# Kernel tuning notes

Hardware: AMD Instinct MI355X
Metric: run time of the kernel (lower is better)

Reference implementation:

```python
import jax, jax.numpy as jnp
import numpy as np

L, B, S, D, H, F, V = 6, 4, 512, 768, 12, 3072, 30522
DH = D // H
EPS = 1e-12
SCALE = 1.0 / float(np.sqrt(DH))


def _ln(x, g, b):
    m = jnp.mean(x, axis=-1, keepdims=True)
    v = jnp.mean(jnp.square(x - m), axis=-1, keepdims=True)
    return (x - m) * jax.lax.rsqrt(v + EPS) * g + b


def _mha(xq, xkv, Wq, bq, Wk, bk, Wv, bv, causal):
    Bc, Sq, _ = xq.shape
    Sk = xkv.shape[1]
    q = (xq @ Wq + bq).reshape(Bc, Sq, H, DH).transpose(0, 2, 1, 3)
    k = (xkv @ Wk + bk).reshape(Bc, Sk, H, DH).transpose(0, 2, 1, 3)
    v = (xkv @ Wv + bv).reshape(Bc, Sk, H, DH).transpose(0, 2, 1, 3)
    s = jnp.einsum('bhqd,bhkd->bhqk', q, k) * SCALE
    if causal is not None:
        s = jnp.where(causal[None, None], s, -jnp.inf)
    p = jax.nn.softmax(s, axis=-1)
    ctx = jnp.einsum('bhqk,bhkd->bhqd', p, v)
    return ctx.transpose(0, 2, 1, 3).reshape(Bc, Sq, H * DH)


def _fwd(input_ids, encoder_hidden, word_emb, pos_emb, tok_emb, emb_g, emb_b,
         Wq, bq, Wk, bk, Wv, bv, Wo, bo, ln1_g, ln1_b,
         cWq, cbq, cWk, cbk, cWv, cbv, cWo, cbo, ln2_g, ln2_b,
         Wi, bi, Wf, bf, ln3_g, ln3_b,
         Wt, bt, lnh_g, lnh_b, Wdec, bdec):
    Bc, Sc = input_ids.shape
    # BertEmbeddings: word + position + token_type(all zeros) -> LayerNorm
    h = word_emb[input_ids] + pos_emb[:Sc][None] + tok_emb[0][None, None]
    h = _ln(h, emb_g, emb_b)
    causal = jnp.tril(jnp.ones((Sc, Sc), dtype=bool))
    for l in range(L):
        # causal self-attention + residual LayerNorm
        ctx = _mha(h, h, Wq[l], bq[l], Wk[l], bk[l], Wv[l], bv[l], causal)
        h = _ln(h + ctx @ Wo[l] + bo[l], ln1_g[l], ln1_b[l])
        # cross-attention over encoder_hidden (no mask) + residual LayerNorm
        ctx = _mha(h, encoder_hidden, cWq[l], cbq[l], cWk[l], cbk[l], cWv[l], cbv[l], None)
        h = _ln(h + ctx @ cWo[l] + cbo[l], ln2_g[l], ln2_b[l])
        # FFN (erf-gelu) + residual LayerNorm
        ff = jax.nn.gelu(h @ Wi[l] + bi[l], approximate=False) @ Wf[l] + bf[l]
        h = _ln(h + ff, ln3_g[l], ln3_b[l])
    # BertOnlyMLMHead: transform (dense+gelu+LN) then vocab projection
    t = _ln(jax.nn.gelu(h @ Wt + bt, approximate=False), lnh_g, lnh_b)
    return t @ Wdec + bdec


def setup_inputs() -> dict:
    keys = iter(jax.random.split(jax.random.key(0), 64))
    def rn(shape, s=0.02):
        return jax.random.normal(next(keys), shape, jnp.float32) * s
    inp = {
        'input_ids': jax.random.randint(next(keys), (B, S), 0, V),
        'encoder_hidden': jax.random.normal(next(keys), (B, S, D), jnp.float32),
        'word_emb': rn((V, D)), 'pos_emb': rn((S, D)), 'tok_emb': rn((2, D)),
        'emb_g': jnp.ones((D,), jnp.float32), 'emb_b': jnp.zeros((D,), jnp.float32),
        'Wq': rn((L, D, D)), 'bq': jnp.zeros((L, D), jnp.float32),
        'Wk': rn((L, D, D)), 'bk': jnp.zeros((L, D), jnp.float32),
        'Wv': rn((L, D, D)), 'bv': jnp.zeros((L, D), jnp.float32),
        'Wo': rn((L, D, D)), 'bo': jnp.zeros((L, D), jnp.float32),
        'ln1_g': jnp.ones((L, D), jnp.float32), 'ln1_b': jnp.zeros((L, D), jnp.float32),
        'cWq': rn((L, D, D)), 'cbq': jnp.zeros((L, D), jnp.float32),
        'cWk': rn((L, D, D)), 'cbk': jnp.zeros((L, D), jnp.float32),
        'cWv': rn((L, D, D)), 'cbv': jnp.zeros((L, D), jnp.float32),
        'cWo': rn((L, D, D)), 'cbo': jnp.zeros((L, D), jnp.float32),
        'ln2_g': jnp.ones((L, D), jnp.float32), 'ln2_b': jnp.zeros((L, D), jnp.float32),
        'Wi': rn((L, D, F)), 'bi': jnp.zeros((L, F), jnp.float32),
        'Wf': rn((L, F, D)), 'bf': jnp.zeros((L, D), jnp.float32),
        'ln3_g': jnp.ones((L, D), jnp.float32), 'ln3_b': jnp.zeros((L, D), jnp.float32),
        'Wt': rn((D, D)), 'bt': jnp.zeros((D,), jnp.float32),
        'lnh_g': jnp.ones((D,), jnp.float32), 'lnh_b': jnp.zeros((D,), jnp.float32),
        'Wdec': rn((D, V)), 'bdec': jnp.zeros((V,), jnp.float32),
    }
    return inp


def reference(input_ids, encoder_hidden, word_emb, pos_emb, tok_emb, emb_g, emb_b,
              Wq, bq, Wk, bk, Wv, bv, Wo, bo, ln1_g, ln1_b,
              cWq, cbq, cWk, cbk, cWv, cbv, cWo, cbo, ln2_g, ln2_b,
              Wi, bi, Wf, bf, ln3_g, ln3_b,
              Wt, bt, lnh_g, lnh_b, Wdec, bdec):
    return _fwd(input_ids, encoder_hidden, word_emb, pos_emb, tok_emb, emb_g, emb_b,
                Wq, bq, Wk, bk, Wv, bv, Wo, bo, ln1_g, ln1_b,
                cWq, cbq, cWk, cbk, cWv, cbv, cWo, cbo, ln2_g, ln2_b,
                Wi, bi, Wf, bf, ln3_g, ln3_b,
                Wt, bt, lnh_g, lnh_b, Wdec, bdec)
```

## Files before the change

### kernel.cpp

```cpp
#include <hip/hip_runtime.h>
#include <math.h>

typedef unsigned short u16;
typedef unsigned int   u32;
typedef long long      i64;
typedef __attribute__((ext_vector_type(8))) __bf16 bf16x8;
typedef __attribute__((ext_vector_type(4))) float  f32x4;
typedef __attribute__((ext_vector_type(8))) u16    u16x8;
typedef __attribute__((ext_vector_type(4))) u16    u16x4;

#define LN_EPS 1e-12f

__device__ __forceinline__ float b2f(u16 u){ union {u32 i; float f;} v; v.i = ((u32)u)<<16; return v.f; }
__device__ __forceinline__ u16 f2b(float f){ union {float f; u32 i;} v; v.f = f; u32 r = v.i + 0x7FFFu + ((v.i>>16)&1u); return (u16)(r>>16); }

__device__ __forceinline__ void gl2lds16(const u16* g, u16* l) {
  __builtin_amdgcn_global_load_lds((const __attribute__((address_space(1))) void*)g,
                                   (__attribute__((address_space(3))) void*)l, 16, 0, 0);
}

struct GemmArgs {
  const u16* A; const u16* Bt; void* C;
  const float* bias0; const float* bias1; const float* bias2;
  int lda, ldb, ldc, M, N, K, bias_seg, act, cf32;
};

template<int BM, int BN, int WM, int WN>
__global__ __launch_bounds__(WM*WN*64)
void gemm_bt2(GemmArgs g) {
  constexpr int NTHR = WM*WN*64;
  constexpr int MI = BM/(WM*16);
  constexpr int NJ = BN/(WN*16);
  constexpr int RA = (BM*4)/NTHR;
  constexpr int RB = (BN*4)/NTHR;
  __shared__ u16 As[2][BM*32];
  __shared__ u16 Bs[2][BN*32];
  const int tid  = threadIdx.x;
  const int wave = tid >> 6, lane = tid & 63;
  const int wm = wave / WN, wn = wave % WN;
  const int lrow = lane & 15, quad = lane >> 4;

  int bx, by;
  {
    const int gx = gridDim.x;
    const int nwg = gx * gridDim.y;
    const int wg = blockIdx.y * gx + blockIdx.x;
    if (nwg >= 512) {
      const int q = nwg >> 3, r = nwg & 7;
      const int xcd = wg & 7, loc = wg >> 3;
      const int nid = (xcd < r ? xcd * (q + 1) : r * (q + 1) + (xcd - r) * q) + loc;
      bx = nid % gx; by = nid / gx;
    } else { bx = blockIdx.x; by = blockIdx.y; }
  }

  const u16* Ab = g.A + (i64)bx*BM*g.lda;
  const u16* Bt = g.Bt;
  const int n0 = by * BN;

  const int srow = tid >> 2;
  const int sps  = tid & 3;

  f32x4 acc[MI][NJ];
  #pragma unroll
  for (int i=0;i<MI;i++)
    #pragma unroll
    for (int j=0;j<NJ;j++) acc[i][j] = (f32x4){0.f,0.f,0.f,0.f};

  auto stage = [&](int buf, int k0) {
    #pragma unroll
    for (int la=0; la<RA; ++la) {
      int row = la*(NTHR>>2) + srow;
      int ls = sps ^ ((row>>1)&3);
      const u16* src = Ab + (i64)row*g.lda + k0 + (ls<<3);
      gl2lds16(src, &As[buf][(la*NTHR + (wave<<6))<<3]);
    }
    #pragma unroll
    for (int la=0; la<RB; ++la) {
      int row = la*(NTHR>>2) + srow;
      int nrow = n0 + row; if (nrow >= g.N) nrow = g.N-1;
      int ls = sps ^ ((row>>1)&3);
      const u16* src = Bt + (i64)nrow*g.ldb + k0 + (ls<<3);
      gl2lds16(src, &Bs[buf][(la*NTHR + (wave<<6))<<3]);
    }
  };

  const int NT = g.K >> 5;
  stage(0, 0);
  __syncthreads();
  for (int t = 0; t < NT; ++t) {
    const int cur = t & 1;
    if (t+1 < NT) stage(cur^1, (t+1)<<5);
    const int xr = (lrow>>1)&3;
    bf16x8 a[MI], b[NJ];
    #pragma unroll
    for (int i=0;i<MI;i++) {
      int r = wm*(MI*16) + i*16 + lrow;
      a[i] = *(const bf16x8*)&As[cur][r*32 + ((quad^xr)<<3)];
    }
    #pragma unroll
    for (int j=0;j<NJ;j++) {
      int r = wn*(NJ*16) + j*16 + lrow;
      b[j] = *(const bf16x8*)&Bs[cur][r*32 + ((quad^xr)<<3)];
    }
    #pragma unroll
    for (int i=0;i<MI;i++)
      #pragma unroll
      for (int j=0;j<NJ;j++)
        acc[i][j] = __builtin_amdgcn_mfma_f32_16x16x32_bf16(a[i], b[j], acc[i][j], 0,0,0);
    __syncthreads();
  }

  const i64 rowbase = (i64)bx*BM + wm*(MI*16);
  u16*   Cb = (u16*)g.C;
  float* Cf = (float*)g.C;
  #pragma unroll
  for (int i=0;i<MI;i++) {
    #pragma unroll
    for (int j=0;j<NJ;j++) {
      int col = n0 + wn*(NJ*16) + (j<<4) + lrow;
      if (col < g.N) {
        float bias = 0.f;
        if (g.bias0) {
          int seg = col / g.bias_seg;
          const float* bp = (seg==0) ? g.bias0 : ((seg==1) ? g.bias1 : g.bias2);
          bias = bp[col - seg*g.bias_seg];
        }
        #pragma unroll
        for (int r=0;r<4;r++) {
          i64 row = rowbase + (i<<4) + (quad<<2) + r;
          float v = acc[i][j][r] + bias;
          if (g.act == 1) v = 0.5f*v*(1.0f + erff(v*0.70710678118654752f));
          if (g.cf32) Cf[row*(i64)g.ldc + col] = v;
          else        Cb[row*(i64)g.ldc + col] = f2b(v);
        }
      }
    }
  }
}

__global__ __launch_bounds__(64) void flash_attn(const u16* __restrict__ qkv,
                                                 const u16* __restrict__ VT,
                                                 u16* __restrict__ ctx, int causal) {
  const int lane = threadIdx.x & 63;
  const int qi = lane & 15, g = lane >> 4;
  const int q0 = blockIdx.x << 4;
  const int bh = blockIdx.y;
  const int b = bh / 12, h = bh % 12;
  const int q = q0 + qi;

  const u16* Qp = qkv + (i64)(b*512 + q)*2304 + h*64 + (g<<3);
  bf16x8 qf0 = *(const bf16x8*)Qp;
  bf16x8 qf1 = *(const bf16x8*)(Qp + 32);

  const u16* Kp = qkv + ((i64)(b*512 + qi))*2304 + 768 + h*64 + (g<<3);
  const u16* Vp = VT + (i64)bh*32768 + (i64)qi*512 + (g<<3);

  f32x4 o[4];
  #pragma unroll
  for (int s=0;s<4;s++) o[s] = (f32x4){0.f,0.f,0.f,0.f};
  float m = -1e30f, lsum = 0.f;

  const int sA = qi + ((g & 1) << 5);
  const int sB = sA + 16;
  const int tsel = g >> 1;

  const int nt = causal ? (q0 >> 6) + 1 : 8;
  for (int kt = 0; kt < nt; ++kt) {
    const int kv0 = kt << 6;

    bf16x8 kf[4][2];
    #pragma unroll
    for (int t=0;t<4;t++)
      #pragma unroll
      for (int w=0;w<2;w++)
        kf[t][w] = *(const bf16x8*)(Kp + (i64)(kv0 + (t<<4))*2304 + (w<<5));
    bf16x8 vf[4][2];
    #pragma unroll
    for (int s=0;s<4;s++)
      #pragma unroll
      for (int w=0;w<2;w++)
        vf[s][w] = *(const bf16x8*)(Vp + (s<<13) + kv0 + (w<<5));

    f32x4 sc[4];
    #pragma unroll
    for (int t=0;t<4;t++) {
      sc[t] = (f32x4){0.f,0.f,0.f,0.f};
      sc[t] = __builtin_amdgcn_mfma_f32_16x16x32_bf16(kf[t][0], qf0, sc[t], 0,0,0);
      sc[t] = __builtin_amdgcn_mfma_f32_16x16x32_bf16(kf[t][1], qf1, sc[t], 0,0,0);
    }

    float x[4][4];
    #pragma unroll
    for (int t=0;t<4;t++)
      #pragma unroll
      for (int r=0;r<4;r++) {
        float v = sc[t][r] * 0.125f;
        int key = kv0 + (t<<4) + (g<<2) + r;
        if (causal && key > q) v = -1e30f;
        x[t][r] = v;
      }

    float mt = x[0][0];
    #pragma unroll
    for (int t=0;t<4;t++)
      #pragma unroll
      for (int r=0;r<4;r++) mt = fmaxf(mt, x[t][r]);
    mt = fmaxf(mt, __shfl_xor(mt, 16));
    mt = fmaxf(mt, __shfl_xor(mt, 32));
    float mn = fmaxf(m, mt);
    float c = __expf(m - mn);
    m = mn;

    float p[4][4];
    float ps = 0.f;
    #pragma unroll
    for (int t=0;t<4;t++)
      #pragma unroll
      for (int r=0;r<4;r++) { float e = __expf(x[t][r] - mn); p[t][r] = e; ps += e; }
    ps += __shfl_xor(ps, 16);
    ps += __shfl_xor(ps, 32);
    lsum = lsum * c + ps;
    #pragma unroll
    for (int s=0;s<4;s++) o[s] *= c;

    u32 pkLo[4], pkHi[4];
    #pragma unroll
    for (int t=0;t<4;t++) {
      pkLo[t] = (u32)f2b(p[t][0]) | ((u32)f2b(p[t][1]) << 16);
      pkHi[t] = (u32)f2b(p[t][2]) | ((u32)f2b(p[t][3]) << 16);
    }

    #pragma unroll
    for (int w=0;w<2;w++) {
      u32 w0=0, w1=0, w2=0, w3=0;
      #pragma unroll
      for (int tl=0; tl<2; ++tl) {
        const int t = 2*w + tl;
        u32 aLo = (u32)__shfl((int)pkLo[t], sA);
        u32 aHi = (u32)__shfl((int)pkHi[t], sA);
        u32 bLo = (u32)__shfl((int)pkLo[t], sB);
        u32 bHi = (u32)__shfl((int)pkHi[t], sB);
        if (tsel == tl) { w0=aLo; w1=aHi; w2=bLo; w3=bHi; }
      }
      union { bf16x8 v; u32 u[4]; } pf;
      pf.u[0]=w0; pf.u[1]=w1; pf.u[2]=w2; pf.u[3]=w3;
      #pragma unroll
      for (int s=0;s<4;s++)
        o[s] = __builtin_amdgcn_mfma_f32_16x16x32_bf16(vf[s][w], pf.v, o[s], 0,0,0);
    }
  }

  float inv = 1.0f / lsum;
  u16* orow = ctx + (i64)(b*512 + q)*768 + h*64 + (g<<2);
  #pragma unroll
  for (int s=0;s<4;s++) {
    u16x4 ov;
    #pragma unroll
    for (int r=0;r<4;r++) ov[r] = f2b(o[s][r] * inv);
    *(u16x4*)(orow + (s<<4)) = ov;
  }
}

__device__ __forceinline__ float block_reduce_sum_256(float v, float* red) {
  #pragma unroll
  for (int off=32; off; off>>=1) v += __shfl_xor(v, off);
  int wave = threadIdx.x >> 6;
  __syncthreads();
  if ((threadIdx.x & 63) == 0) red[wave] = v;
  __syncthreads();
  return red[0]+red[1]+red[2]+red[3];
}

__global__ __launch_bounds__(256) void resln_kernel(const float* base, const float* delta,
                                                    const float* gam, const float* bet,
                                                    float* out_f, u16* out_b) {
  __shared__ float red[4];
  i64 off = (i64)blockIdx.x * 768;
  int tid = threadIdx.x;
  float x[3];
  #pragma unroll
  for (int j=0;j<3;j++) {
    int i = tid + j*256;
    float v = delta[off+i];
    if (base) v += base[off+i];
    x[j] = v;
  }
  float s = block_reduce_sum_256(x[0]+x[1]+x[2], red);
  float mean = s * (1.0f/768.0f);
  float q = 0.f;
  #pragma unroll
  for (int j=0;j<3;j++) { float d = x[j]-mean; q += d*d; }
  q = block_reduce_sum_256(q, red);
  float r = rsqrtf(q*(1.0f/768.0f) + LN_EPS);
  #pragma unroll
  for (int j=0;j<3;j++) {
    int i = tid + j*256;
    float y = (x[j]-mean)*r*gam[i] + bet[i];
    out_f[off+i] = y;
    out_b[off+i] = f2b(y);
  }
}

__global__ __launch_bounds__(256) void embed_kernel(const int* ids, const float* wemb,
    const float* pemb, const float* temb, const float* gam, const float* bet,
    float* out_f, u16* out_b) {
  __shared__ float red[4];
  int row = blockIdx.x;
  int s = row & 511;
  i64 wrow = (i64)ids[row] * 768;
  i64 off = (i64)row * 768;
  int tid = threadIdx.x;
  float x[3];
  #pragma unroll
  for (int j=0;j<3;j++) {
    int i = tid + j*256;
    x[j] = wemb[wrow+i] + pemb[(i64)s*768+i] + temb[i];
  }
  float sm = block_reduce_sum_256(x[0]+x[1]+x[2], red);
  float mean = sm * (1.0f/768.0f);
  float q = 0.f;
  #pragma unroll
  for (int j=0;j<3;j++) { float d = x[j]-mean; q += d*d; }
  q = block_reduce_sum_256(q, red);
  float r = rsqrtf(q*(1.0f/768.0f) + LN_EPS);
  #pragma unroll
  for (int j=0;j<3;j++) {
    int i = tid + j*256;
    float y = (x[j]-mean)*r*gam[i] + bet[i];
    out_f[off+i] = y;
    out_b[off+i] = f2b(y);
  }
}

__global__ __launch_bounds__(256) void cvt_kernel(const float* src, u16* dst, int n) {
  int i = (blockIdx.x*256 + threadIdx.x) * 4;
  if (i + 3 < n) {
    float4 v = *(const float4*)&src[i];
    dst[i+0]=f2b(v.x); dst[i+1]=f2b(v.y); dst[i+2]=f2b(v.z); dst[i+3]=f2b(v.w);
  }
}

struct TransEntry { const float* src; u16* dst; int K, N, tile0; };
struct TransArgs  { TransEntry e[12]; int n; };

__global__ __launch_bounds__(256) void transpose_multi(TransArgs ta) {
  __shared__ u16 tile[64][72];
  int t = blockIdx.x;
  int ei = 0;
  for (int i=1;i<ta.n;i++) if (t >= ta.e[i].tile0) ei = i;
  TransEntry E = ta.e[ei];
  int lt = t - E.tile0;
  int ntn = (E.N + 63) >> 6;
  int tk = lt / ntn, tn = lt - tk*ntn;
  int tid = threadIdx.x;
  int kk = tid >> 2, c = (tid & 3) << 4;
  i64 gk = (i64)(tk*64 + kk);
  int gn0 = tn*64 + c;
  const float* srow = E.src + gk * E.N;
  if (gn0 + 16 <= E.N) {
    #pragma unroll
    for (int j=0;j<16;j++) tile[kk][c+j] = f2b(srow[gn0+j]);
  } else {
    for (int j=0;j<16;j++) tile[kk][c+j] = (gn0+j < E.N) ? f2b(srow[gn0+j]) : (u16)0;
  }
  __syncthreads();
  int nn = tid >> 2, kc = (tid & 3) << 4;
  int gn = tn*64 + nn;
  if (gn < E.N) {
    u16x8 v0, v1;
    #pragma unroll
    for (int j=0;j<8;j++) { v0[j] = tile[kc+j][nn]; v1[j] = tile[kc+8+j][nn]; }
    u16* drow = E.dst + (i64)gn*E.K + tk*64 + kc;
    *(u16x8*)&drow[0] = v0;
    *(u16x8*)&drow[8] = v1;
  }
}

__global__ __launch_bounds__(256) void vtrans_kernel(const u16* qkv, u16* VT) {
  __shared__ u16 tile[64][72];
  int bh = blockIdx.z; int b = bh / 12, hh = bh % 12;
  const u16* src = qkv + (i64)b*512*2304 + 1536 + hh*64;
  u16* dst = VT + (i64)bh*64*512;
  int kt = blockIdx.x;
  int tid = threadIdx.x;
  int kk = tid >> 2, c = (tid & 3) << 4;
  const u32* p = (const u32*)&src[(i64)(kt*64+kk)*2304 + c];
  #pragma unroll
  for (int j=0;j<8;j++) *(u32*)&tile[kk][c + 2*j] = p[j];
  __syncthreads();
  int dd = tid >> 2, kc = (tid & 3) << 4;
  u16x8 v0, v1;
  #pragma unroll
  for (int j=0;j<8;j++) { v0[j] = tile[kc+j][dd]; v1[j] = tile[kc+8+j][dd]; }
  u16* drow = dst + (i64)dd*512 + kt*64 + kc;
  *(u16x8*)&drow[0] = v0;
  *(u16x8*)&drow[8] = v1;
}

static void gemm_args(GemmArgs& g, const u16* A, int lda, const u16* Bt, int ldb,
                      void* C, int ldc, int M, int N, int K, const float* b0,
                      const float* b1, const float* b2, int bias_seg, int act, int cf32) {
  g.A=A; g.Bt=Bt; g.C=C; g.bias0=b0; g.bias1=b1; g.bias2=b2;
  g.lda=lda; g.ldb=ldb; g.ldc=ldc; g.M=M; g.N=N; g.K=K;
  g.bias_seg=bias_seg; g.act=act; g.cf32=cf32;
}

static void g2_128(const u16* A, int lda, const u16* Bt, int ldb, void* C, int ldc,
                   int M, int N, int K, const float* b0, const float* b1, const float* b2,
                   int bias_seg, int act, int cf32, hipStream_t st) {
  GemmArgs g; gemm_args(g, A, lda, Bt, ldb, C, ldc, M, N, K, b0, b1, b2, bias_seg, act, cf32);
  gemm_bt2<128,128,2,2><<<dim3(M/128, (N+127)/128), 256, 0, st>>>(g);
}

static void g2_64(const u16* A, int lda, const u16* Bt, int ldb, void* C, int ldc,
                  int M, int N, int K, const float* b0, const float* b1, const float* b2,
                  int bias_seg, int act, int cf32, hipStream_t st) {
  GemmArgs g; gemm_args(g, A, lda, Bt, ldb, C, ldc, M, N, K, b0, b1, b2, bias_seg, act, cf32);
  gemm_bt2<64,128,1,2><<<dim3(M/64, (N+127)/128), 128, 0, st>>>(g);
}

static void g2_256(const u16* A, int lda, const u16* Bt, int ldb, void* C, int ldc,
                   int M, int N, int K, const float* b0, const float* b1, const float* b2,
                   int bias_seg, int act, int cf32, hipStream_t st) {
  GemmArgs g; gemm_args(g, A, lda, Bt, ldb, C, ldc, M, N, K, b0, b1, b2, bias_seg, act, cf32);
  gemm_bt2<256,256,2,4><<<dim3(M/256, (N+255)/256), 512, 0, st>>>(g);
}

extern "C" void kernel_launch(void* const* d_in, const int* in_sizes, int n_in,
                              void* d_out, int out_size, void* d_ws, size_t ws_size,
                              hipStream_t stream) {
  (void)in_sizes; (void)n_in; (void)out_size;
  const int*   ids  = (const int*)d_in[0];
  const float* enc  = (const float*)d_in[1];
  const float* wemb = (const float*)d_in[2];
  const float* pemb = (const float*)d_in[3];
  const float* temb = (const float*)d_in[4];
  const float* eg   = (const float*)d_in[5];
  const float* eb   = (const float*)d_in[6];
  const float* Wq=(const float*)d_in[7];  const float* bq=(const float*)d_in[8];
  const float* Wk=(const float*)d_in[9];  const float* bk=(const float*)d_in[10];
  const float* Wv=(const float*)d_in[11]; const float* bv=(const float*)d_in[12];
  const float* Wo=(const float*)d_in[13]; const float* bo=(const float*)d_in[14];
  const float* l1g=(const float*)d_in[15]; const float* l1b=(const float*)d_in[16];
  const float* cWq=(const float*)d_in[17]; const float* cbq=(const float*)d_in[18];
  const float* cWk=(const float*)d_in[19]; const float* cbk=(const float*)d_in[20];
  const float* cWv=(const float*)d_in[21]; const float* cbv=(const float*)d_in[22];
  const float* cWo=(const float*)d_in[23]; const float* cbo=(const float*)d_in[24];
  const float* l2g=(const float*)d_in[25]; const float* l2b=(const float*)d_in[26];
  const float* Wi=(const float*)d_in[27];  const float* bi=(const float*)d_in[28];
  const float* Wf=(const float*)d_in[29];  const float* bff=(const float*)d_in[30];
  const float* l3g=(const float*)d_in[31]; const float* l3b=(const float*)d_in[32];
  const float* Wt=(const float*)d_in[33];  const float* bt=(const float*)d_in[34];
  const float* lhg=(const float*)d_in[35]; const float* lhb=(const float*)d_in[36];
  const float* Wdec=(const float*)d_in[37]; const float* bdec=(const float*)d_in[38];
  float* out = (float*)d_out;

  u16* ws     = (u16*)d_ws;
  u16* WT     = ws;
  u16* h_bf   = WT + 24030720;
  float* h_f  = (float*)(h_bf + 1572864);
  float* h2_f = h_f + 1572864;
  u16* qkv    = (u16*)(h2_f + 1572864);
  u16* ctx    = qkv + 4718592;
  u16* VT     = ctx + 1572864;
  u16* enc_bf = VT + 1572864;
  u16* Smat   = enc_bf + 1572864;
  u16* mid    = Smat;
  if (ws_size < (size_t)53915136 * 2) return;

  const int DD = 589824, DF = 2359296;
  u16* qkvT = WT;
  u16* woT  = WT + 1769472;
  u16* cqT  = WT + 2359296;
  u16* ckvT = WT + 2949120;
  u16* cwoT = WT + 4128768;
  u16* wiT  = WT + 4718592;
  u16* wfT  = WT + 7077888;

  embed_kernel<<<2048, 256, 0, stream>>>(ids, wemb, pemb, temb, eg, eb, h_f, h_bf);
  cvt_kernel<<<1536, 256, 0, stream>>>(enc, enc_bf, 1572864);

  for (int l = 0; l < 6; l++) {
    TransArgs ta; int tile = 0; int idx = 0;
    auto add = [&](const float* s, u16* d, int K, int N) {
      ta.e[idx].src=s; ta.e[idx].dst=d; ta.e[idx].K=K; ta.e[idx].N=N; ta.e[idx].tile0=tile;
      tile += (K/64)*((N+63)/64); idx++;
    };
    add(Wq +(i64)l*DD, qkvT,        768, 768);
    add(Wk +(i64)l*DD, qkvT+DD,     768, 768);
    add(Wv +(i64)l*DD, qkvT+2*DD,   768, 768);
    add(Wo +(i64)l*DD, woT,         768, 768);
    add(cWq+(i64)l*DD, cqT,         768, 768);
    add(cWk+(i64)l*DD, ckvT,        768, 768);
    add(cWv+(i64)l*DD, ckvT+DD,     768, 768);
    add(cWo+(i64)l*DD, cwoT,        768, 768);
    add(Wi +(i64)l*DF, wiT,         768, 3072);
    add(Wf +(i64)l*DF, wfT,         3072, 768);
    ta.n = idx;
    transpose_multi<<<tile, 256, 0, stream>>>(ta);

    g2_128(h_bf, 768, qkvT, 768, qkv, 2304, 2048, 2304, 768,
           bq+l*768, bk+l*768, bv+l*768, 768, 0, 0, stream);
    vtrans_kernel<<<dim3(8,1,48), 256, 0, stream>>>(qkv, VT);
    flash_attn<<<dim3(32,48), 64, 0, stream>>>(qkv, VT, ctx, 1);
    g2_64(ctx, 768, woT, 768, h2_f, 768, 2048, 768, 768,
          bo+l*768, nullptr, nullptr, 768, 0, 1, stream);
    resln_kernel<<<2048, 256, 0, stream>>>(h_f, h2_f, l1g+l*768, l1b+l*768, h_f, h_bf);

    g2_64(h_bf, 768, cqT, 768, qkv, 2304, 2048, 768, 768,
          cbq+l*768, nullptr, nullptr, 768, 0, 0, stream);
    g2_64(enc_bf, 768, ckvT, 768, qkv+768, 2304, 2048, 1536, 768,
          cbk+l*768, cbv+l*768, nullptr, 768, 0, 0, stream);
    vtrans_kernel<<<dim3(8,1,48), 256, 0, stream>>>(qkv, VT);
    flash_attn<<<dim3(32,48), 64, 0, stream>>>(qkv, VT, ctx, 0);
    g2_64(ctx, 768, cwoT, 768, h2_f, 768, 2048, 768, 768,
          cbo+l*768, nullptr, nullptr, 768, 0, 1, stream);
    resln_kernel<<<2048, 256, 0, stream>>>(h_f, h2_f, l2g+l*768, l2b+l*768, h_f, h_bf);

    g2_128(h_bf, 768, wiT, 768, mid, 3072, 2048, 3072, 768,
           bi+l*3072, nullptr, nullptr, 3072, 1, 0, stream);
    g2_64(mid, 3072, wfT, 3072, h2_f, 768, 2048, 768, 3072,
          bff+l*768, nullptr, nullptr, 768, 0, 1, stream);
    resln_kernel<<<2048, 256, 0, stream>>>(h_f, h2_f, l3g+l*768, l3b+l*768, h_f, h_bf);
  }

  u16* wtT   = WT;
  u16* wdecT = WT + 589824;
  {
    TransArgs ta; int tile = 0; int idx = 0;
    auto add = [&](const float* s, u16* d, int K, int N) {
      ta.e[idx].src=s; ta.e[idx].dst=d; ta.e[idx].K=K; ta.e[idx].N=N; ta.e[idx].tile0=tile;
      tile += (K/64)*((N+63)/64); idx++;
    };
    add(Wt,   wtT,   768, 768);
    add(Wdec, wdecT, 768, 30522);
    ta.n = idx;
    transpose_multi<<<tile, 256, 0, stream>>>(ta);
  }
  g2_64(h_bf, 768, wtT, 768, h2_f, 768, 2048, 768, 768, bt, nullptr, nullptr, 768, 1, 1, stream);
  resln_kernel<<<2048, 256, 0, stream>>>(nullptr, h2_f, lhg, lhb, h_f, h_bf);
  g2_256(h_bf, 768, wdecT, 768, out, 30522, 2048, 30522, 768,
         bdec, nullptr, nullptr, 30522, 0, 1, stream);
}
```

Baseline: 2.532 ms.

## Triple-buffer GEMM LDS staging with explicit vmcnt waits; use 128 tiles for decoder

The GEMM kernel moves from double to triple LDS buffering and prefetches two K-steps ahead. The old full __syncthreads is replaced by s_waitcnt vmcnt waits plus raw barriers, so global-to-LDS loads can overlap more compute. The vocab projection now uses 128x128 tiles instead of 256x256. The extra buffer raises LDS use, which may lower occupancy, and the hand-written waitcnt and barrier placement must be exactly right for correctness.

```diff
diff --git a/kernel.cpp b/kernel.cpp
--- a/kernel.cpp
+++ b/kernel.cpp
@@ -19,6 +19,13 @@
                                    (__attribute__((address_space(3))) void*)l, 16, 0, 0);
 }
 
+template<int N> __device__ __forceinline__ void vm_wait() {
+  asm volatile("s_waitcnt vmcnt(%0)" :: "i"(N) : "memory");
+}
+__device__ __forceinline__ void lgkm0() {
+  asm volatile("s_waitcnt lgkmcnt(0)" ::: "memory");
+}
+
 struct GemmArgs {
   const u16* A; const u16* Bt; void* C;
   const float* bias0; const float* bias1; const float* bias2;
@@ -27,14 +34,15 @@
 
 template<int BM, int BN, int WM, int WN>
 __global__ __launch_bounds__(WM*WN*64)
-void gemm_bt2(GemmArgs g) {
+void gemm_bt3(GemmArgs g) {
   constexpr int NTHR = WM*WN*64;
   constexpr int MI = BM/(WM*16);
   constexpr int NJ = BN/(WN*16);
   constexpr int RA = (BM*4)/NTHR;
   constexpr int RB = (BN*4)/NTHR;
-  __shared__ u16 As[2][BM*32];
-  __shared__ u16 Bs[2][BN*32];
+  constexpr int L  = RA+RB;
+  __shared__ u16 As[3][BM*32];
+  __shared__ u16 Bs[3][BN*32];
   const int tid  = threadIdx.x;
   const int wave = tid >> 6, lane = tid & 63;
   const int wm = wave / WN, wn = wave % WN;
@@ -86,10 +94,14 @@
 
   const int NT = g.K >> 5;
   stage(0, 0);
-  __syncthreads();
+  if (NT > 1) stage(1, 32);
   for (int t = 0; t < NT; ++t) {
-    const int cur = t & 1;
-    if (t+1 < NT) stage(cur^1, (t+1)<<5);
+    const int cur = t % 3;
+    if (t+2 < NT) { stage((t+2)%3, (t+2)<<5); vm_wait<2*L>(); }
+    else if (t+1 < NT) { vm_wait<L>(); }
+    else { vm_wait<0>(); }
+    __builtin_amdgcn_s_barrier();
+    __builtin_amdgcn_sched_barrier(0);
     const int xr = (lrow>>1)&3;
     bf16x8 a[MI], b[NJ];
     #pragma unroll
@@ -102,12 +114,14 @@
       int r = wn*(NJ*16) + j*16 + lrow;
       b[j] = *(const bf16x8*)&Bs[cur][r*32 + ((quad^xr)<<3)];
     }
+    lgkm0();
+    __builtin_amdgcn_s_barrier();
+    __builtin_amdgcn_sched_barrier(0);
     #pragma unroll
     for (int i=0;i<MI;i++)
       #pragma unroll
       for (int j=0;j<NJ;j++)
         acc[i][j] = __builtin_amdgcn_mfma_f32_16x16x32_bf16(a[i], b[j], acc[i][j], 0,0,0);
-    __syncthreads();
   }
 
   const i64 rowbase = (i64)bx*BM + wm*(MI*16);
@@ -405,25 +419,18 @@
   g.bias_seg=bias_seg; g.act=act; g.cf32=cf32;
 }
 
-static void g2_128(const u16* A, int lda, const u16* Bt, int ldb, void* C, int ldc,
+static void g3_128(const u16* A, int lda, const u16* Bt, int ldb, void* C, int ldc,
                    int M, int N, int K, const float* b0, const float* b1, const float* b2,
                    int bias_seg, int act, int cf32, hipStream_t st) {
   GemmArgs g; gemm_args(g, A, lda, Bt, ldb, C, ldc, M, N, K, b0, b1, b2, bias_seg, act, cf32);
-  gemm_bt2<128,128,2,2><<<dim3(M/128, (N+127)/128), 256, 0, st>>>(g);
-}
-
-static void g2_64(const u16* A, int lda, const u16* Bt, int ldb, void* C, int ldc,
+  gemm_bt3<128,128,2,2><<<dim3(M/128, (N+127)/128), 256, 0, st>>>(g);
+}
+
+static void g3_64(const u16* A, int lda, const u16* Bt, int ldb, void* C, int ldc,
                   int M, int N, int K, const float* b0, const float* b1, const float* b2,
                   int bias_seg, int act, int cf32, hipStream_t st) {
   GemmArgs g; gemm_args(g, A, lda, Bt, ldb, C, ldc, M, N, K, b0, b1, b2, bias_seg, act, cf32);
-  gemm_bt2<64,128,1,2><<<dim3(M/64, (N+127)/128), 128, 0, st>>>(g);
-}
-
-static void g2_256(const u16* A, int lda, const u16* Bt, int ldb, void* C, int ldc,
-                   int M, int N, int K, const float* b0, const float* b1, const float* b2,
-                   int bias_seg, int act, int cf32, hipStream_t st) {
-  GemmArgs g; gemm_args(g, A, lda, Bt, ldb, C, ldc, M, N, K, b0, b1, b2, bias_seg, act, cf32);
-  gemm_bt2<256,256,2,4><<<dim3(M/256, (N+255)/256), 512, 0, st>>>(g);
+  gemm_bt3<64,128,1,2><<<dim3(M/64, (N+127)/128), 128, 0, st>>>(g);
 }
 
 extern "C" void kernel_launch(void* const* d_in, const int* in_sizes, int n_in,
@@ -499,27 +506,27 @@
     ta.n = idx;
     transpose_multi<<<tile, 256, 0, stream>>>(ta);
 
-    g2_128(h_bf, 768, qkvT, 768, qkv, 2304, 2048, 2304, 768,
+    g3_128(h_bf, 768, qkvT, 768, qkv, 2304, 2048, 2304, 768,
            bq+l*768, bk+l*768, bv+l*768, 768, 0, 0, stream);
     vtrans_kernel<<<dim3(8,1,48), 256, 0, stream>>>(qkv, VT);
     flash_attn<<<dim3(32,48), 64, 0, stream>>>(qkv, VT, ctx, 1);
-    g2_64(ctx, 768, woT, 768, h2_f, 768, 2048, 768, 768,
+    g3_64(ctx, 768, woT, 768, h2_f, 768, 2048, 768, 768,
           bo+l*768, nullptr, nullptr, 768, 0, 1, stream);
     resln_kernel<<<2048, 256, 0, stream>>>(h_f, h2_f, l1g+l*768, l1b+l*768, h_f, h_bf);
 
-    g2_64(h_bf, 768, cqT, 768, qkv, 2304, 2048, 768, 768,
+    g3_64(h_bf, 768, cqT, 768, qkv, 2304, 2048, 768, 768,
           cbq+l*768, nullptr, nullptr, 768, 0, 0, stream);
-    g2_64(enc_bf, 768, ckvT, 768, qkv+768, 2304, 2048, 1536, 768,
+    g3_64(enc_bf, 768, ckvT, 768, qkv+768, 2304, 2048, 1536, 768,
           cbk+l*768, cbv+l*768, nullptr, 768, 0, 0, stream);
     vtrans_kernel<<<dim3(8,1,48), 256, 0, stream>>>(qkv, VT);
     flash_attn<<<dim3(32,48), 64, 0, stream>>>(qkv, VT, ctx, 0);
-    g2_64(ctx, 768, cwoT, 768, h2_f, 768, 2048, 768, 768,
+    g3_64(ctx, 768, cwoT, 768, h2_f, 768, 2048, 768, 768,
           cbo+l*768, nullptr, nullptr, 768, 0, 1, stream);
     resln_kernel<<<2048, 256, 0, stream>>>(h_f, h2_f, l2g+l*768, l2b+l*768, h_f, h_bf);
 
-    g2_128(h_bf, 768, wiT, 768, mid, 3072, 2048, 3072, 768,
+    g3_128(h_bf, 768, wiT, 768, mid, 3072, 2048, 3072, 768,
            bi+l*3072, nullptr, nullptr, 3072, 1, 0, stream);
-    g2_64(mid, 3072, wfT, 3072, h2_f, 768, 2048, 768, 3072,
+    g3_64(mid, 3072, wfT, 3072, h2_f, 768, 2048, 768, 3072,
           bff+l*768, nullptr, nullptr, 768, 0, 1, stream);
     resln_kernel<<<2048, 256, 0, stream>>>(h_f, h2_f, l3g+l*768, l3b+l*768, h_f, h_bf);
   }
@@ -537,8 +544,8 @@
     ta.n = idx;
     transpose_multi<<<tile, 256, 0, stream>>>(ta);
   }
-  g2_64(h_bf, 768, wtT, 768, h2_f, 768, 2048, 768, 768, bt, nullptr, nullptr, 768, 1, 1, stream);
+  g3_64(h_bf, 768, wtT, 768, h2_f, 768, 2048, 768, 768, bt, nullptr, nullptr, 768, 1, 1, stream);
   resln_kernel<<<2048, 256, 0, stream>>>(nullptr, h2_f, lhg, lhb, h_f, h_bf);
-  g2_256(h_bf, 768, wdecT, 768, out, 30522, 2048, 30522, 768,
+  g3_128(h_bf, 768, wdecT, 768, out, 30522, 2048, 30522, 768,
          bdec, nullptr, nullptr, 30522, 0, 1, stream);
 }
```

Result: no change. 2.507 ms (-1.0%).
